# Optimization experiments

Measured on AMD Instinct MI355X. Metric: run time of the kernel, lower is better.

Reference implementation:

```python
import jax, jax.numpy as jnp
import numpy as np

EPS = 1e-5
SLOPE = 0.01  # torch LeakyReLU default

def _conv(x, w, b, stride):
    # x: [B,C,L], w: [O,I,3]
    y = jax.lax.conv_general_dilated(x, w, (stride,), [(1, 1)],
                                     dimension_numbers=("NCH", "OIH", "NCH"))
    return y + b[None, :, None]

def _bn(x, g, b, m, v):
    # eval-mode BatchNorm1d with running stats
    inv = jax.lax.rsqrt(v + EPS)
    return (x - m[None, :, None]) * (g * inv)[None, :, None] + b[None, :, None]

def _lrelu(x):
    return jnp.where(x >= 0, x, SLOPE * x)

def setup_inputs() -> dict:
    key = jax.random.key(0)
    ks = jax.random.split(key, 32)
    B, C, L = 32, 256, 2048
    K, D = 4096, 128
    d = {}
    d["x"] = jax.random.normal(ks[0], (B, C, L), dtype=jnp.float32)
    # conv weights [O,I,3]
    d["w1"] = jax.random.normal(ks[1], (256, 256, 3), jnp.float32) * 0.03
    d["b1"] = jax.random.normal(ks[2], (256,), jnp.float32) * 0.01
    d["w2"] = jax.random.normal(ks[3], (512, 256, 3), jnp.float32) * 0.03
    d["b2"] = jax.random.normal(ks[4], (512,), jnp.float32) * 0.01
    d["w3"] = jax.random.normal(ks[5], (512, 512, 3), jnp.float32) * 0.02
    d["b3"] = jax.random.normal(ks[6], (512,), jnp.float32) * 0.01
    d["w4"] = jax.random.normal(ks[7], (D, 512, 3), jnp.float32) * 0.02
    d["b4"] = jax.random.normal(ks[8], (D,), jnp.float32) * 0.01
    for i, ch in enumerate([256, 512, 512, D]):
        d[f"g{i+1}"] = 1.0 + 0.1 * jax.random.normal(ks[9 + 4 * i], (ch,), jnp.float32)
        d[f"be{i+1}"] = 0.1 * jax.random.normal(ks[10 + 4 * i], (ch,), jnp.float32)
        d[f"m{i+1}"] = 0.1 * jax.random.normal(ks[11 + 4 * i], (ch,), jnp.float32)
        d[f"v{i+1}"] = 0.5 + jax.random.uniform(ks[12 + 4 * i], (ch,), jnp.float32)
    d["emb"] = jax.random.uniform(ks[30], (K, D), jnp.float32,
                                  minval=-1.0 / K, maxval=1.0 / K)
    return d

def reference(x, w1, b1, w2, b2, w3, b3, w4, b4,
              g1, be1, m1, v1, g2, be2, m2, v2,
              g3, be3, m3, v3, g4, be4, m4, v4, emb):
    h = _lrelu(_bn(_conv(x, w1, b1, 2), g1, be1, m1, v1))   # [B,256,L/2]
    h = _lrelu(_bn(_conv(h, w2, b2, 2), g2, be2, m2, v2))   # [B,512,L/4]
    h = _lrelu(_bn(_conv(h, w3, b3, 2), g3, be3, m3, v3))   # [B,512,L/8]
    h = _lrelu(_bn(_conv(h, w4, b4, 1), g4, be4, m4, v4))   # [B,D,L/8]
    flat = jnp.transpose(h, (0, 2, 1)).reshape(-1, h.shape[1])  # [N,D]
    # squared-distance expansion: ||f||^2 + ||e||^2 - 2 f.e
    dist = (jnp.sum(flat * flat, axis=1, keepdims=True)
            + jnp.sum(emb * emb, axis=1)
            - 2.0 * flat @ emb.T)                            # [N,K]
    codes = jnp.argmin(dist, axis=1)
    return codes, dist
```

## Files before the change

kernel.cpp:

```cpp
#include <hip/hip_runtime.h>
#include <cstdint>
#include <math.h>

#define EPS_BN 1e-5f
#define SLOPE 0.01f
#define C14 6.103515625e-5f
#define SC14 16384.0f
#define HMIN 6.103515625e-5f

typedef __attribute__((ext_vector_type(8))) _Float16 half8;
typedef __attribute__((ext_vector_type(8))) short short8;
typedef __attribute__((ext_vector_type(16))) float f32x16;
typedef __attribute__((ext_vector_type(4))) float f32x4;

__device__ __forceinline__ void split16(float v, unsigned short& uh,
                                        unsigned short& ul) {
    _Float16 h = (_Float16)v;
    if (fabsf(v) < HMIN) h = (_Float16)0.0f;
    float rem = v - (float)h;
    _Float16 l = (_Float16)(rem * SC14);
    uh = __builtin_bit_cast(unsigned short, h);
    ul = __builtin_bit_cast(unsigned short, l);
}

typedef const __attribute__((address_space(1))) unsigned int* gas_ptr;
typedef __attribute__((address_space(3))) unsigned int* las_ptr;
__device__ __forceinline__ void glds16(const void* g, void* l) {
    __builtin_amdgcn_global_load_lds((gas_ptr)g, (las_ptr)l, 16, 0, 0);
}

__global__ __launch_bounds__(256)
void wprep_all(const float* __restrict__ w1, short* __restrict__ o1,
               const float* __restrict__ w2, short* __restrict__ o2,
               const float* __restrict__ w3, short* __restrict__ o3,
               const float* __restrict__ w4, short* __restrict__ o4)
{
    const float* w; short* wbuf; int CIN, COUT;
    switch (blockIdx.y) {
        case 0: w = w1; wbuf = o1; CIN = 256; COUT = 256; break;
        case 1: w = w2; wbuf = o2; CIN = 256; COUT = 512; break;
        case 2: w = w3; wbuf = o3; CIN = 512; COUT = 512; break;
        default: w = w4; wbuf = o4; CIN = 512; COUT = 128; break;
    }
    int KST = CIN / 16, OB = COUT / 128;
    int total = KST * OB * 1536;
    for (int sid = blockIdx.x * 256 + threadIdx.x; sid < total;
         sid += gridDim.x * 256) {
        int slot = sid % 1536;
        int kb = sid / 1536;
        int ob = kb % OB, ks = kb / OB;
        int m = slot & 31, hi = (slot >> 5) & 1, mf = (slot >> 6) & 3;
        int ts = slot >> 8;
        int t = ts >> 1, s = ts & 1;
        int oc = ob * 128 + mf * 32 + m;
        int ib = ks * 16 + hi * 8;
        short8 r;
        #pragma unroll
        for (int j = 0; j < 8; ++j) {
            float v = w[((size_t)oc * CIN + ib + j) * 3 + t];
            unsigned short uh, ul;
            split16(v, uh, ul);
            r[j] = (short)(s == 0 ? uh : ul);
        }
        *(short8*)(wbuf + (size_t)sid * 8) = r;
    }
}

__global__ __launch_bounds__(256)
void bnprep_init(
    const float* __restrict__ g1, const float* __restrict__ be1,
    const float* __restrict__ m1, const float* __restrict__ v1,
    const float* __restrict__ b1, float* __restrict__ sc1, float* __restrict__ off1,
    const float* __restrict__ g2, const float* __restrict__ be2,
    const float* __restrict__ m2, const float* __restrict__ v2,
    const float* __restrict__ b2, float* __restrict__ sc2, float* __restrict__ off2,
    const float* __restrict__ g3, const float* __restrict__ be3,
    const float* __restrict__ m3, const float* __restrict__ v3,
    const float* __restrict__ b3, float* __restrict__ sc3, float* __restrict__ off3,
    const float* __restrict__ g4, const float* __restrict__ be4,
    const float* __restrict__ m4, const float* __restrict__ v4,
    const float* __restrict__ b4, float* __restrict__ sc4, float* __restrict__ off4,
    unsigned long long* __restrict__ mp)
{
    int bid = blockIdx.x;
    if (bid >= 6) {
        mp[(bid - 6) * 256 + threadIdx.x] = ~0ULL;
        return;
    }
    const float *g, *be, *m, *v, *bias;
    float *sc, *off;
    int c;
    if (bid == 0) {
        g = g1; be = be1; m = m1; v = v1; bias = b1; sc = sc1; off = off1;
        c = threadIdx.x;
    } else if (bid <= 2) {
        g = g2; be = be2; m = m2; v = v2; bias = b2; sc = sc2; off = off2;
        c = (bid - 1) * 256 + threadIdx.x;
    } else if (bid <= 4) {
        g = g3; be = be3; m = m3; v = v3; bias = b3; sc = sc3; off = off3;
        c = (bid - 3) * 256 + threadIdx.x;
    } else {
        g = g4; be = be4; m = m4; v = v4; bias = b4; sc = sc4; off = off4;
        c = threadIdx.x;
        if (c >= 128) return;
    }
    float s = g[c] / sqrtf(v[c] + EPS_BN);
    sc[c] = s;
    off[c] = (bias[c] - m[c]) * s + be[c];
}

__global__ __launch_bounds__(256)
void xsplit(const float* __restrict__ x, short* __restrict__ xpl)
{
    const size_t PL = (size_t)32 * 32 * 2 * 1025 * 8;
    int l = blockIdx.x * 256 + threadIdx.x;
    int g = blockIdx.y, b = blockIdx.z;
    float v[8];
    #pragma unroll
    for (int j = 0; j < 8; ++j)
        v[j] = x[((size_t)b * 256 + g * 8 + j) * 2048 + l];
    int arr = l & 1;
    int slot = arr ? (l + 1) / 2 : l / 2 + 1;
    size_t base = ((((size_t)b * 32 + g) * 2 + arr) * 1025 + slot) * 8;
    short8 rh, rl;
    #pragma unroll
    for (int j = 0; j < 8; ++j) {
        unsigned short uh, ul;
        split16(v[j], uh, ul);
        rh[j] = (short)uh; rl[j] = (short)ul;
    }
    *(short8*)(xpl + base) = rh;
    *(short8*)(xpl + PL + base) = rl;
    if (l == 0) {
        short8 z;
        #pragma unroll
        for (int j = 0; j < 8; ++j) z[j] = 0;
        for (int sg = 0; sg < 2; ++sg)
            for (int a2 = 0; a2 < 2; ++a2)
                *(short8*)(xpl + sg * PL +
                           ((((size_t)b * 32 + g) * 2 + a2) * 1025) * 8) = z;
    }
}

template<int CIN, int COUT, int LIN, int STRIDE, int EPI>
__global__ __launch_bounds__(256, 2)
void conv_mfma(const short* __restrict__ wbuf, const short* __restrict__ xpl,
               const float* __restrict__ scv, const float* __restrict__ offv,
               short* __restrict__ opl, float* __restrict__ fout)
{
    constexpr int LOUT = LIN / STRIDE;
    constexpr int KST = CIN / 16;
    constexpr int OB = COUT / 128;
    constexpr int NG = CIN / 8;
    constexpr int NARR = (STRIDE == 2) ? 2 : 1;
    constexpr int SLOTS = (STRIDE == 2) ? (LIN / 2 + 1) : (LIN + 2);
    constexpr size_t PLIN = (size_t)32 * NG * NARR * SLOTS * 8;
    constexpr int NGo = COUT / 8;
    constexpr int OSLOTS = (EPI == 0) ? (LOUT / 2 + 1) : (LOUT + 2);
    constexpr size_t PLOUT = (size_t)32 * NGo * ((EPI == 0) ? 2 : 1) * OSLOTS * 8;

    constexpr int XOFF = 24576;
    constexpr int BUF  = 41472;
    constexpr int SCOFF = BUF;
    __shared__ __align__(16) char lds[BUF + 1024];

    const int tid = threadIdx.x;
    const int lane = tid & 63;
    const int wv = tid >> 6;
    const int wm = wv >> 1, wn = wv & 1;
    const int hi = lane >> 5, n32 = lane & 31;
    const int n0 = blockIdx.x * 128;
    const int ob = blockIdx.y;
    const int o0 = ob * 128;
    const int b = blockIdx.z;

    if (tid < 128) {
        ((float*)(lds + SCOFF))[tid] = scv[o0 + tid];
        ((float*)(lds + SCOFF + 512))[tid] = offv[o0 + tid];
    }

    f32x16 acc0[2][2], acc1[2][2];
    #pragma unroll
    for (int i = 0; i < 2; ++i)
        #pragma unroll
        for (int j = 0; j < 2; ++j)
            #pragma unroll
            for (int e = 0; e < 16; ++e) { acc0[i][j][e] = 0.0f; acc1[i][j][e] = 0.0f; }

    const short* wg = wbuf + (size_t)ob * 1536 * 8;
    const int lanexoff = hi * 4224 + n32 * 16;

    #pragma unroll 1
    for (int ks = 0; ks < KST; ++ks) {
        __syncthreads();
        {
            const short* wsrc = wg + (size_t)ks * OB * 1536 * 8;
            #pragma unroll
            for (int it = 0; it < 6; ++it) {
                int slot0 = it * 256 + wv * 64;
                glds16(wsrc + (size_t)(slot0 + lane) * 8, lds + slot0 * 16);
            }
        }
        {
            int g0 = ks * 2;
            constexpr int NRUNS = (STRIDE == 2) ? 8 : 4;
            for (int r = wv; r < NRUNS; r += 4) {
                int sg, rhi, arr, start, cnt;
                if (STRIDE == 2) {
                    sg = r >> 2; rhi = (r >> 1) & 1; arr = r & 1;
                    start = arr ? n0 : (n0 + 1);
                    cnt = arr ? 129 : 128;
                } else {
                    sg = r >> 1; rhi = r & 1; arr = 0;
                    start = n0; cnt = 130;
                }
                const short* src = xpl + (size_t)sg * PLIN
                    + ((((size_t)b * NG + (g0 + rhi)) * NARR + arr) * SLOTS + start) * 8;
                char* dst = lds + XOFF + ((sg * 2 + rhi) * 2 + arr) * 2112;
                for (int c0 = 0; c0 < cnt; c0 += 64) {
                    if (lane < cnt - c0)
                        glds16(src + (size_t)(c0 + lane) * 8, dst + c0 * 16);
                }
            }
        }
        __syncthreads();
        #pragma unroll
        for (int t = 0; t < 3; ++t) {
            half8 af[2][2], bx[2][2];
            #pragma unroll
            for (int s = 0; s < 2; ++s) {
                #pragma unroll
                for (int mf = 0; mf < 2; ++mf)
                    af[s][mf] = *(const half8*)(lds +
                        (((t * 2 + s) * 4 + (wm * 2 + mf)) * 64 + lane) * 16);
                #pragma unroll
                for (int nf = 0; nf < 2; ++nf) {
                    int arr, qb;
                    if (STRIDE == 2) {
                        arr = (t == 1) ? 0 : 1;
                        qb = wn * 64 + nf * 32 + ((t == 2) ? 1 : 0);
                    } else {
                        arr = 0;
                        qb = wn * 64 + nf * 32 + t;
                    }
                    bx[s][nf] = *(const half8*)(lds + XOFF + s * 8448
                                                + arr * 2112 + qb * 16 + lanexoff);
                }
            }
            #pragma unroll
            for (int mf = 0; mf < 2; ++mf)
                #pragma unroll
                for (int nf = 0; nf < 2; ++nf) {
                    acc0[mf][nf] = __builtin_amdgcn_mfma_f32_32x32x16_f16(
                        af[0][mf], bx[0][nf], acc0[mf][nf], 0, 0, 0);
                    acc1[mf][nf] = __builtin_amdgcn_mfma_f32_32x32x16_f16(
                        af[0][mf], bx[1][nf], acc1[mf][nf], 0, 0, 0);
                    acc1[mf][nf] = __builtin_amdgcn_mfma_f32_32x32x16_f16(
                        af[1][mf], bx[0][nf], acc1[mf][nf], 0, 0, 0);
                }
        }
    }

    #pragma unroll
    for (int half = 0; half < 2; ++half) {
        __syncthreads();
        #pragma unroll
        for (int mf = 0; mf < 2; ++mf)
            #pragma unroll
            for (int r = 0; r < 16; ++r) {
                int ocl = mf * 32 + (r & 3) + 8 * (r >> 2) + 4 * hi;
                *(float*)(lds + wv * 8704 + n32 * 272 + ocl * 4) =
                    acc0[mf][half][r] + C14 * acc1[mf][half][r];
            }
        __syncthreads();
        #pragma unroll
        for (int it = 0; it < 4; ++it) {
            int sl = tid + it * 256;
            int w = sl >> 8, rem = sl & 255, p = rem >> 3, grp = rem & 7;
            int wm_ = w >> 1, wn_ = w & 1;
            f32x4 v0 = *(f32x4*)(lds + w * 8704 + p * 272 + grp * 32);
            f32x4 v1 = *(f32x4*)(lds + w * 8704 + p * 272 + grp * 32 + 16);
            int oclb = wm_ * 64 + grp * 8;
            f32x4 s0 = *(f32x4*)(lds + SCOFF + oclb * 4);
            f32x4 s1 = *(f32x4*)(lds + SCOFF + oclb * 4 + 16);
            f32x4 q0 = *(f32x4*)(lds + SCOFF + 512 + oclb * 4);
            f32x4 q1 = *(f32x4*)(lds + SCOFF + 512 + oclb * 4 + 16);
            float y[8];
            #pragma unroll
            for (int j = 0; j < 4; ++j) {
                float a = v0[j] * s0[j] + q0[j];
                y[j] = a >= 0.0f ? a : SLOPE * a;
                float c = v1[j] * s1[j] + q1[j];
                y[4 + j] = c >= 0.0f ? c : SLOPE * c;
            }
            int pos_abs = n0 + wn_ * 64 + half * 32 + p;
            int oc_abs = o0 + oclb;
            if (EPI == 2) {
                f32x4 w0, w1;
                #pragma unroll
                for (int j = 0; j < 4; ++j) { w0[j] = y[j]; w1[j] = y[4 + j]; }
                float* fp = fout + ((size_t)(b * 256 + pos_abs)) * 128 + oc_abs;
                *(f32x4*)fp = w0;
                *(f32x4*)(fp + 4) = w1;
            } else {
                short8 rh, rl;
                #pragma unroll
                for (int j = 0; j < 8; ++j) {
                    unsigned short uh, ul;
                    split16(y[j], uh, ul);
                    rh[j] = (short)uh; rl[j] = (short)ul;
                }
                int gq = oc_abs >> 3;
                size_t base;
                if (EPI == 0) {
                    int arr = pos_abs & 1;
                    int slot = arr ? (pos_abs + 1) / 2 : pos_abs / 2 + 1;
                    base = ((((size_t)b * NGo + gq) * 2 + arr) * OSLOTS + slot) * 8;
                } else {
                    base = (((size_t)b * NGo + gq) * OSLOTS + (pos_abs + 1)) * 8;
                }
                *(short8*)(opl + base) = rh;
                *(short8*)(opl + PLOUT + base) = rl;
            }
        }
    }

    if (EPI == 0) {
        if (blockIdx.x == 0 && tid < 64) {
            int sg = tid / 32, r2 = tid % 32, g16 = r2 >> 1, a2 = r2 & 1;
            int gq = ob * 16 + g16;
            short8 z;
            #pragma unroll
            for (int j = 0; j < 8; ++j) z[j] = 0;
            *(short8*)(opl + (size_t)sg * PLOUT +
                       ((((size_t)b * NGo + gq) * 2 + a2) * OSLOTS) * 8) = z;
        }
    } else if (EPI == 1) {
        if (tid < 32 && (blockIdx.x == 0 || blockIdx.x == gridDim.x - 1)) {
            int sg = tid / 16, g16 = tid % 16;
            int gq = ob * 16 + g16;
            int slot = (blockIdx.x == 0) ? 0 : (OSLOTS - 1);
            short8 z;
            #pragma unroll
            for (int j = 0; j < 8; ++j) z[j] = 0;
            *(short8*)(opl + (size_t)sg * PLOUT +
                       (((size_t)b * NGo + gq) * OSLOTS + slot) * 8) = z;
        }
    }
}

__global__ __launch_bounds__(256)
void split_kernel(const float* __restrict__ src, int nrows,
                  short* __restrict__ ph, short* __restrict__ pl,
                  float* __restrict__ sumv)
{
    int t = blockIdx.x * 256 + threadIdx.x;
    int n = t >> 4, g = t & 15;
    if (n >= nrows) return;
    const float* rowp = src + (size_t)n * 128 + g * 8;
    float4 v0 = *(const float4*)rowp;
    float4 v1 = *(const float4*)(rowp + 4);
    float vv[8] = {v0.x, v0.y, v0.z, v0.w, v1.x, v1.y, v1.z, v1.w};
    short8 rh, rl;
    float ss = 0.0f;
    #pragma unroll
    for (int j = 0; j < 8; ++j) {
        float v = vv[j];
        ss = fmaf(v, v, ss);
        unsigned short uh, ul;
        split16(v, uh, ul);
        rh[j] = (short)uh; rl[j] = (short)ul;
    }
    int nb = n >> 5, m = n & 31, ks = g >> 1, hi = g & 1;
    size_t slot = ((((size_t)nb * 8 + ks) * 2 + hi) * 32 + m) * 8;
    *(short8*)(ph + slot) = rh;
    *(short8*)(pl + slot) = rl;
    #pragma unroll
    for (int mk = 8; mk; mk >>= 1) ss += __shfl_xor(ss, mk);
    if (g == 0) sumv[n] = ss;
}

__global__ __launch_bounds__(256, 2)
void distmin_kernel(const short* __restrict__ fh, const short* __restrict__ fl,
                    const short* __restrict__ eh, const short* __restrict__ el,
                    const float* __restrict__ sf, const float* __restrict__ se,
                    float* __restrict__ dist, unsigned long long* __restrict__ mp)
{
    __shared__ unsigned long long cand[128 * 64];
    const int tid = threadIdx.x;
    const int lane = tid & 63;
    const int wv = tid >> 6;
    const int wm = wv >> 1, wn = wv & 1;
    const int hi = lane >> 5, n32 = lane & 31;
    const int kb = blockIdx.x;
    const int nb = blockIdx.y;

    f32x16 acc0[2][2], acc1[2][2];
    #pragma unroll
    for (int i = 0; i < 2; ++i)
        #pragma unroll
        for (int j = 0; j < 2; ++j)
            #pragma unroll
            for (int e = 0; e < 16; ++e) { acc0[i][j][e] = 0.0f; acc1[i][j][e] = 0.0f; }

    const short* fb[2][2];
    const short* eb[2][2];
    {
        const short* fpl[2] = {fh, fl};
        const short* epl[2] = {eh, el};
        #pragma unroll
        for (int s = 0; s < 2; ++s) {
            #pragma unroll
            for (int mf = 0; mf < 2; ++mf)
                fb[s][mf] = fpl[s] + (size_t)nb * 16384
                            + ((size_t)(wm * 2 + mf) * 8 * 64 + lane) * 8;
            #pragma unroll
            for (int nf = 0; nf < 2; ++nf)
                eb[s][nf] = epl[s]
                            + ((size_t)(kb * 4 + wn * 2 + nf) * 8 * 64 + lane) * 8;
        }
    }

    #pragma unroll
    for (int ks = 0; ks < 8; ++ks) {
        half8 af[2][2], bx[2][2];
        #pragma unroll
        for (int s = 0; s < 2; ++s) {
            #pragma unroll
            for (int mf = 0; mf < 2; ++mf)
                af[s][mf] = *(const half8*)(fb[s][mf] + ks * 512);
            #pragma unroll
            for (int nf = 0; nf < 2; ++nf)
                bx[s][nf] = *(const half8*)(eb[s][nf] + ks * 512);
        }
        #pragma unroll
        for (int mf = 0; mf < 2; ++mf)
            #pragma unroll
            for (int nf = 0; nf < 2; ++nf) {
                acc0[mf][nf] = __builtin_amdgcn_mfma_f32_32x32x16_f16(
                    af[0][mf], bx[0][nf], acc0[mf][nf], 0, 0, 0);
                acc1[mf][nf] = __builtin_amdgcn_mfma_f32_32x32x16_f16(
                    af[0][mf], bx[1][nf], acc1[mf][nf], 0, 0, 0);
                acc1[mf][nf] = __builtin_amdgcn_mfma_f32_32x32x16_f16(
                    af[1][mf], bx[0][nf], acc1[mf][nf], 0, 0, 0);
            }
    }

    const int n_blk = nb * 128;
    const int kc0 = kb * 128 + wn * 64 + n32;
    const float se0 = se[kc0];
    const float se1 = se[kc0 + 32];
    #pragma unroll
    for (int mf = 0; mf < 2; ++mf) {
        #pragma unroll
        for (int r = 0; r < 16; ++r) {
            int nloc = wm * 64 + mf * 32 + (r & 3) + 8 * (r >> 2) + 4 * hi;
            int n = n_blk + nloc;
            float sfn = sf[n];
            float d0 = acc0[mf][0][r] + C14 * acc1[mf][0][r];
            float d1 = acc0[mf][1][r] + C14 * acc1[mf][1][r];
            float v0 = (sfn + se0) - 2.0f * d0;
            float v1 = (sfn + se1) - 2.0f * d1;
            dist[(size_t)n * 4096 + kc0] = v0;
            dist[(size_t)n * 4096 + kc0 + 32] = v1;
            unsigned long long p0 =
                (((unsigned long long)__float_as_uint(v0)) << 32) | (unsigned)kc0;
            unsigned long long p1 =
                (((unsigned long long)__float_as_uint(v1)) << 32) | (unsigned)(kc0 + 32);
            unsigned long long p = p1 < p0 ? p1 : p0;
            cand[nloc * 64 + wn * 32 + n32] = p;
        }
    }
    __syncthreads();
    {
        int row = tid >> 1, h = tid & 1;
        unsigned long long best = ~0ULL;
        #pragma unroll
        for (int i = 0; i < 32; ++i) {
            int c = h * 32 + ((i + row) & 31);
            unsigned long long cv = cand[row * 64 + c];
            best = cv < best ? cv : best;
        }
        unsigned lo = (unsigned)best, hw = (unsigned)(best >> 32);
        unsigned lo2 = __shfl_xor(lo, 1), hw2 = __shfl_xor(hw, 1);
        unsigned long long ob = (((unsigned long long)hw2) << 32) | lo2;
        if (ob < best) best = ob;
        if (h == 0) atomicMin(mp + n_blk + row, best);
    }
}

__global__ __launch_bounds__(256)
void codes_kernel(const unsigned long long* __restrict__ mp,
                  float* __restrict__ codes)
{
    int n = blockIdx.x * 256 + threadIdx.x;
    if (n < 8192) codes[n] = (float)(unsigned)(mp[n] & 0xffffffffULL);
}

extern "C" void kernel_launch(void* const* d_in, const int* in_sizes, int n_in,
                              void* d_out, int out_size, void* d_ws, size_t ws_size,
                              hipStream_t stream)
{
    const float* x   = (const float*)d_in[0];
    const float* w1  = (const float*)d_in[1];
    const float* b1  = (const float*)d_in[2];
    const float* w2  = (const float*)d_in[3];
    const float* b2  = (const float*)d_in[4];
    const float* w3  = (const float*)d_in[5];
    const float* b3  = (const float*)d_in[6];
    const float* w4  = (const float*)d_in[7];
    const float* b4  = (const float*)d_in[8];
    const float* g1  = (const float*)d_in[9];
    const float* be1 = (const float*)d_in[10];
    const float* m1  = (const float*)d_in[11];
    const float* v1  = (const float*)d_in[12];
    const float* g2  = (const float*)d_in[13];
    const float* be2 = (const float*)d_in[14];
    const float* m2  = (const float*)d_in[15];
    const float* v2  = (const float*)d_in[16];
    const float* g3  = (const float*)d_in[17];
    const float* be3 = (const float*)d_in[18];
    const float* m3  = (const float*)d_in[19];
    const float* v3  = (const float*)d_in[20];
    const float* g4  = (const float*)d_in[21];
    const float* be4 = (const float*)d_in[22];
    const float* m4  = (const float*)d_in[23];
    const float* v4  = (const float*)d_in[24];
    const float* emb = (const float*)d_in[25];

    float* outf  = (float*)d_out;
    float* codes = outf;
    float* distm = outf + 8192;

    char* wsb = (char*)d_ws;
    short* wb1 = (short*)(wsb + 0);
    short* wb2 = (short*)(wsb + 786432);
    short* wb3 = (short*)(wsb + 2359296);
    short* wb4 = (short*)(wsb + 5505024);
    float* sc1 = (float*)(wsb + 6291456); float* off1 = sc1 + 256;
    float* sc2 = (float*)(wsb + 6293504); float* off2 = sc2 + 512;
    float* sc3 = (float*)(wsb + 6297600); float* off3 = sc3 + 512;
    float* sc4 = (float*)(wsb + 6301696); float* off4 = sc4 + 128;
    short* h1p = (short*)(wsb + 6302720);
    short* fh  = (short*)(wsb + 39922688);
    short* fl  = (short*)(wsb + 42019840);
    short* eh  = (short*)(wsb + 44116992);
    short* el  = (short*)(wsb + 45165568);
    float* sf  = (float*)(wsb + 46214144);
    float* se  = (float*)(wsb + 46246912);
    unsigned long long* mp = (unsigned long long*)(wsb + 46263296);

    char* db = (char*)distm;
    short* xpl = (short*)db;
    short* h2p = (short*)db;
    short* h3p = (short*)(db + 33685504);
    float* f   = (float*)(db + 80000000);

    wprep_all<<<dim3(192, 4), 256, 0, stream>>>(w1, wb1, w2, wb2, w3, wb3, w4, wb4);
    bnprep_init<<<38, 256, 0, stream>>>(
        g1, be1, m1, v1, b1, sc1, off1,
        g2, be2, m2, v2, b2, sc2, off2,
        g3, be3, m3, v3, b3, sc3, off3,
        g4, be4, m4, v4, b4, sc4, off4, mp);
    split_kernel<<<256, 256, 0, stream>>>(emb, 4096, eh, el, se);

    xsplit<<<dim3(8, 32, 32), 256, 0, stream>>>(x, xpl);
    conv_mfma<256, 256, 2048, 2, 0>
        <<<dim3(8, 2, 32), 256, 0, stream>>>(wb1, xpl, sc1, off1, h1p, nullptr);
    conv_mfma<256, 512, 1024, 2, 0>
        <<<dim3(4, 4, 32), 256, 0, stream>>>(wb2, h1p, sc2, off2, h2p, nullptr);
    conv_mfma<512, 512, 512, 2, 1>
        <<<dim3(2, 4, 32), 256, 0, stream>>>(wb3, h2p, sc3, off3, h3p, nullptr);
    conv_mfma<512, 128, 256, 1, 2>
        <<<dim3(2, 1, 32), 256, 0, stream>>>(wb4, h3p, sc4, off4, nullptr, f);

    split_kernel<<<512, 256, 0, stream>>>(f, 8192, fh, fl, sf);
    distmin_kernel<<<dim3(32, 64), 256, 0, stream>>>(fh, fl, eh, el,
                                                     sf, se, distm, mp);
    codes_kernel<<<32, 256, 0, stream>>>(mp, codes);
}
```

Baseline: 263.5 us.

## Pair output-channel blocks in 512-thread conv blocks to share input tiles

```diff
diff --git a/kernel.cpp b/kernel.cpp
--- a/kernel.cpp
+++ b/kernel.cpp
@@ -142,22 +142,200 @@
     }
 }
 
-template<int CIN, int COUT, int LIN, int STRIDE, int EPI>
+template<int CIN, int COUT, int LIN, int TILE, int EPI>
+__global__ __launch_bounds__(512, 1)
+void conv_pair(const short* __restrict__ wbuf, const short* __restrict__ xpl,
+               const float* __restrict__ scv, const float* __restrict__ offv,
+               short* __restrict__ opl)
+{
+    constexpr int LOUT = LIN / 2;
+    constexpr int KST = CIN / 16;
+    constexpr int OBS = COUT / 128;
+    constexpr int NG = CIN / 8;
+    constexpr int SLOTS = LIN / 2 + 1;
+    constexpr size_t PLIN = (size_t)32 * NG * 2 * SLOTS * 8;
+    constexpr int NF = TILE / 64;
+    constexpr int NGo = COUT / 8;
+    constexpr int OSLOTS = (EPI == 0) ? (LOUT / 2 + 1) : (LOUT + 2);
+    constexpr size_t PLOUT = (size_t)32 * NGo * ((EPI == 0) ? 2 : 1) * OSLOTS * 8;
+
+    constexpr int XOFF = 49152;
+    constexpr int SCOFF = 69632;
+    __shared__ __align__(16) char lds[71680];
+
+    const int tid = threadIdx.x;
+    const int lane = tid & 63;
+    const int wv = tid >> 6;
+    const int wo = wv >> 2;
+    const int wm = (wv >> 1) & 1, wn = wv & 1;
+    const int hi = lane >> 5, n32 = lane & 31;
+    const int n0 = blockIdx.x * TILE;
+    const int oby = blockIdx.y;
+    const int o0 = oby * 256;
+    const int b = blockIdx.z;
+
+    if (tid < 256) ((float*)(lds + SCOFF))[tid] = scv[o0 + tid];
+    else ((float*)(lds + SCOFF + 1024))[tid - 256] = offv[o0 + tid - 256];
+
+    f32x16 acc0[2][2], acc1[2][2];
+    #pragma unroll
+    for (int i = 0; i < 2; ++i)
+        #pragma unroll
+        for (int j = 0; j < 2; ++j)
+            #pragma unroll
+            for (int e = 0; e < 16; ++e) { acc0[i][j][e] = 0.0f; acc1[i][j][e] = 0.0f; }
+
+    #pragma unroll 1
+    for (int ks = 0; ks < KST; ++ks) {
+        __syncthreads();
+        {
+            const short* wsrc = wbuf +
+                ((size_t)ks * OBS + (oby * 2 + wo)) * 1536 * 8;
+            #pragma unroll
+            for (int it = 0; it < 6; ++it) {
+                int slot0 = it * 256 + (wv & 3) * 64;
+                glds16(wsrc + (size_t)(slot0 + lane) * 8,
+                       lds + wo * 24576 + slot0 * 16);
+            }
+        }
+        {
+            int g0 = ks * 2;
+            int r = wv;
+            int sg = r >> 2, rhi = (r >> 1) & 1, arr = r & 1;
+            int start = arr ? n0 : (n0 + 1);
+            int cnt = arr ? (TILE + 1) : TILE;
+            const short* src = xpl + (size_t)sg * PLIN
+                + ((((size_t)b * NG + (g0 + rhi)) * 2 + arr) * SLOTS + start) * 8;
+            char* dst = lds + XOFF + ((sg * 2 + rhi) * 2 + arr) * 2112;
+            for (int c0 = 0; c0 < cnt; c0 += 64) {
+                if (lane < cnt - c0)
+                    glds16(src + (size_t)(c0 + lane) * 8, dst + c0 * 16);
+            }
+        }
+        __syncthreads();
+        #pragma unroll
+        for (int t = 0; t < 3; ++t) {
+            half8 af[2][2], bx[2][2];
+            #pragma unroll
+            for (int s = 0; s < 2; ++s) {
+                #pragma unroll
+                for (int mf = 0; mf < 2; ++mf)
+                    af[s][mf] = *(const half8*)(lds + wo * 24576 +
+                        (((t * 2 + s) * 4 + (wm * 2 + mf)) * 64 + lane) * 16);
+                int arr = (t == 1) ? 0 : 1;
+                int tof = (t == 2) ? 1 : 0;
+                #pragma unroll
+                for (int nf = 0; nf < NF; ++nf) {
+                    int qb = wn * (TILE / 2) + nf * 32 + tof;
+                    bx[s][nf] = *(const half8*)(lds + XOFF + s * 8448
+                                                + arr * 2112 + qb * 16
+                                                + hi * 4224 + n32 * 16);
+                }
+            }
+            #pragma unroll
+            for (int mf = 0; mf < 2; ++mf)
+                #pragma unroll
+                for (int nf = 0; nf < NF; ++nf) {
+                    acc0[mf][nf] = __builtin_amdgcn_mfma_f32_32x32x16_f16(
+                        af[0][mf], bx[0][nf], acc0[mf][nf], 0, 0, 0);
+                    acc1[mf][nf] = __builtin_amdgcn_mfma_f32_32x32x16_f16(
+                        af[0][mf], bx[1][nf], acc1[mf][nf], 0, 0, 0);
+                    acc1[mf][nf] = __builtin_amdgcn_mfma_f32_32x32x16_f16(
+                        af[1][mf], bx[0][nf], acc1[mf][nf], 0, 0, 0);
+                }
+        }
+    }
+
+    #pragma unroll
+    for (int half = 0; half < NF; ++half) {
+        __syncthreads();
+        #pragma unroll
+        for (int mf = 0; mf < 2; ++mf)
+            #pragma unroll
+            for (int r = 0; r < 16; ++r) {
+                int ocl = mf * 32 + (r & 3) + 8 * (r >> 2) + 4 * hi;
+                *(float*)(lds + wv * 8704 + n32 * 272 + ocl * 4) =
+                    acc0[mf][half][r] + C14 * acc1[mf][half][r];
+            }
+        __syncthreads();
+        #pragma unroll
+        for (int it = 0; it < 4; ++it) {
+            int sl = tid + it * 512;
+            int w = sl >> 8, rem = sl & 255, p = rem >> 3, grp = rem & 7;
+            int wo_ = w >> 2, wm_ = (w >> 1) & 1, wn_ = w & 1;
+            f32x4 v0 = *(f32x4*)(lds + w * 8704 + p * 272 + grp * 32);
+            f32x4 v1 = *(f32x4*)(lds + w * 8704 + p * 272 + grp * 32 + 16);
+            int ocb = wo_ * 128 + wm_ * 64 + grp * 8;
+            f32x4 s0 = *(f32x4*)(lds + SCOFF + ocb * 4);
+            f32x4 s1 = *(f32x4*)(lds + SCOFF + ocb * 4 + 16);
+            f32x4 q0 = *(f32x4*)(lds + SCOFF + 1024 + ocb * 4);
+            f32x4 q1 = *(f32x4*)(lds + SCOFF + 1024 + ocb * 4 + 16);
+            float y[8];
+            #pragma unroll
+            for (int j = 0; j < 4; ++j) {
+                float a = v0[j] * s0[j] + q0[j];
+                y[j] = a >= 0.0f ? a : SLOPE * a;
+                float c = v1[j] * s1[j] + q1[j];
+                y[4 + j] = c >= 0.0f ? c : SLOPE * c;
+            }
+            int pos_abs = n0 + wn_ * (TILE / 2) + half * 32 + p;
+            int oc_abs = o0 + ocb;
+            short8 rh, rl;
+            #pragma unroll
+            for (int j = 0; j < 8; ++j) {
+                unsigned short uh, ul;
+                split16(y[j], uh, ul);
+                rh[j] = (short)uh; rl[j] = (short)ul;
+            }
+            int gq = oc_abs >> 3;
+            size_t base;
+            if (EPI == 0) {
+                int arr = pos_abs & 1;
+                int slot = arr ? (pos_abs + 1) / 2 : pos_abs / 2 + 1;
+                base = ((((size_t)b * NGo + gq) * 2 + arr) * OSLOTS + slot) * 8;
+            } else {
+                base = (((size_t)b * NGo + gq) * OSLOTS + (pos_abs + 1)) * 8;
+            }
+            *(short8*)(opl + base) = rh;
+            *(short8*)(opl + PLOUT + base) = rl;
+        }
+    }
+
+    if (EPI == 0) {
+        if (blockIdx.x == 0 && tid < 128) {
+            int sg = tid >> 6, r2 = tid & 63, g16 = r2 >> 1, a2 = r2 & 1;
+            int gq = oby * 32 + g16;
+            short8 z;
+            #pragma unroll
+            for (int j = 0; j < 8; ++j) z[j] = 0;
+            *(short8*)(opl + (size_t)sg * PLOUT +
+                       ((((size_t)b * NGo + gq) * 2 + a2) * OSLOTS) * 8) = z;
+        }
+    } else {
+        if (tid < 64 && (blockIdx.x == 0 || blockIdx.x == gridDim.x - 1)) {
+            int sg = tid >> 5, g16 = tid & 31;
+            int gq = oby * 32 + g16;
+            int slot = (blockIdx.x == 0) ? 0 : (OSLOTS - 1);
+            short8 z;
+            #pragma unroll
+            for (int j = 0; j < 8; ++j) z[j] = 0;
+            *(short8*)(opl + (size_t)sg * PLOUT +
+                       (((size_t)b * NGo + gq) * OSLOTS + slot) * 8) = z;
+        }
+    }
+}
+
+template<int CIN, int COUT, int LIN>
 __global__ __launch_bounds__(256, 2)
-void conv_mfma(const short* __restrict__ wbuf, const short* __restrict__ xpl,
-               const float* __restrict__ scv, const float* __restrict__ offv,
-               short* __restrict__ opl, float* __restrict__ fout)
-{
-    constexpr int LOUT = LIN / STRIDE;
+void conv_s1(const short* __restrict__ wbuf, const short* __restrict__ xpl,
+             const float* __restrict__ scv, const float* __restrict__ offv,
+             float* __restrict__ fout)
+{
     constexpr int KST = CIN / 16;
     constexpr int OB = COUT / 128;
     constexpr int NG = CIN / 8;
-    constexpr int NARR = (STRIDE == 2) ? 2 : 1;
-    constexpr int SLOTS = (STRIDE == 2) ? (LIN / 2 + 1) : (LIN + 2);
-    constexpr size_t PLIN = (size_t)32 * NG * NARR * SLOTS * 8;
-    constexpr int NGo = COUT / 8;
-    constexpr int OSLOTS = (EPI == 0) ? (LOUT / 2 + 1) : (LOUT + 2);
-    constexpr size_t PLOUT = (size_t)32 * NGo * ((EPI == 0) ? 2 : 1) * OSLOTS * 8;
+    constexpr int SLOTS = LIN + 2;
+    constexpr size_t PLIN = (size_t)32 * NG * SLOTS * 8;
 
     constexpr int XOFF = 24576;
     constexpr int BUF  = 41472;
@@ -203,22 +381,13 @@
         }
         {
             int g0 = ks * 2;
-            constexpr int NRUNS = (STRIDE == 2) ? 8 : 4;
-            for (int r = wv; r < NRUNS; r += 4) {
-                int sg, rhi, arr, start, cnt;
-                if (STRIDE == 2) {
-                    sg = r >> 2; rhi = (r >> 1) & 1; arr = r & 1;
-                    start = arr ? n0 : (n0 + 1);
-                    cnt = arr ? 129 : 128;
-                } else {
-                    sg = r >> 1; rhi = r & 1; arr = 0;
-                    start = n0; cnt = 130;
-                }
+            for (int r = wv; r < 4; r += 4) {
+                int sg = r >> 1, rhi = r & 1;
                 const short* src = xpl + (size_t)sg * PLIN
-                    + ((((size_t)b * NG + (g0 + rhi)) * NARR + arr) * SLOTS + start) * 8;
-                char* dst = lds + XOFF + ((sg * 2 + rhi) * 2 + arr) * 2112;
-                for (int c0 = 0; c0 < cnt; c0 += 64) {
-                    if (lane < cnt - c0)
+                    + (((size_t)b * NG + (g0 + rhi)) * SLOTS + n0) * 8;
+                char* dst = lds + XOFF + (sg * 2 + rhi) * 2112;
+                for (int c0 = 0; c0 < 130; c0 += 64) {
+                    if (lane < 130 - c0)
                         glds16(src + (size_t)(c0 + lane) * 8, dst + c0 * 16);
                 }
             }
@@ -235,16 +404,9 @@
                         (((t * 2 + s) * 4 + (wm * 2 + mf)) * 64 + lane) * 16);
                 #pragma unroll
                 for (int nf = 0; nf < 2; ++nf) {
-                    int arr, qb;
-                    if (STRIDE == 2) {
-                        arr = (t == 1) ? 0 : 1;
-                        qb = wn * 64 + nf * 32 + ((t == 2) ? 1 : 0);
-                    } else {
-                        arr = 0;
-                        qb = wn * 64 + nf * 32 + t;
-                    }
-                    bx[s][nf] = *(const half8*)(lds + XOFF + s * 8448
-                                                + arr * 2112 + qb * 16 + lanexoff);
+                    int qb = wn * 64 + nf * 32 + t;
+                    bx[s][nf] = *(const half8*)(lds + XOFF + s * 4224
+                                                + qb * 16 + hi * 2112 + n32 * 16);
                 }
             }
             #pragma unroll
@@ -285,66 +447,18 @@
             f32x4 s1 = *(f32x4*)(lds + SCOFF + oclb * 4 + 16);
             f32x4 q0 = *(f32x4*)(lds + SCOFF + 512 + oclb * 4);
             f32x4 q1 = *(f32x4*)(lds + SCOFF + 512 + oclb * 4 + 16);
-            float y[8];
+            f32x4 w0, w1;
             #pragma unroll
             for (int j = 0; j < 4; ++j) {
                 float a = v0[j] * s0[j] + q0[j];
-                y[j] = a >= 0.0f ? a : SLOPE * a;
+                w0[j] = a >= 0.0f ? a : SLOPE * a;
                 float c = v1[j] * s1[j] + q1[j];
-                y[4 + j] = c >= 0.0f ? c : SLOPE * c;
+                w1[j] = c >= 0.0f ? c : SLOPE * c;
             }
             int pos_abs = n0 + wn_ * 64 + half * 32 + p;
-            int oc_abs = o0 + oclb;
-            if (EPI == 2) {
-                f32x4 w0, w1;
-                #pragma unroll
-                for (int j = 0; j < 4; ++j) { w0[j] = y[j]; w1[j] = y[4 + j]; }
-                float* fp = fout + ((size_t)(b * 256 + pos_abs)) * 128 + oc_abs;
-                *(f32x4*)fp = w0;
-                *(f32x4*)(fp + 4) = w1;
-            } else {
-                short8 rh, rl;
-                #pragma unroll
-                for (int j = 0; j < 8; ++j) {
-                    unsigned short uh, ul;
-                    split16(y[j], uh, ul);
-                    rh[j] = (short)uh; rl[j] = (short)ul;
-                }
-                int gq = oc_abs >> 3;
-                size_t base;
-                if (EPI == 0) {
-                    int arr = pos_abs & 1;
-                    int slot = arr ? (pos_abs + 1) / 2 : pos_abs / 2 + 1;
-                    base = ((((size_t)b * NGo + gq) * 2 + arr) * OSLOTS + slot) * 8;
-                } else {
-                    base = (((size_t)b * NGo + gq) * OSLOTS + (pos_abs + 1)) * 8;
-                }
-                *(short8*)(opl + base) = rh;
-                *(short8*)(opl + PLOUT + base) = rl;
-            }
-        }
-    }
-
-    if (EPI == 0) {
-        if (blockIdx.x == 0 && tid < 64) {
-            int sg = tid / 32, r2 = tid % 32, g16 = r2 >> 1, a2 = r2 & 1;
-            int gq = ob * 16 + g16;
-            short8 z;
-            #pragma unroll
-            for (int j = 0; j < 8; ++j) z[j] = 0;
-            *(short8*)(opl + (size_t)sg * PLOUT +
-                       ((((size_t)b * NGo + gq) * 2 + a2) * OSLOTS) * 8) = z;
-        }
-    } else if (EPI == 1) {
-        if (tid < 32 && (blockIdx.x == 0 || blockIdx.x == gridDim.x - 1)) {
-            int sg = tid / 16, g16 = tid % 16;
-            int gq = ob * 16 + g16;
-            int slot = (blockIdx.x == 0) ? 0 : (OSLOTS - 1);
-            short8 z;
-            #pragma unroll
-            for (int j = 0; j < 8; ++j) z[j] = 0;
-            *(short8*)(opl + (size_t)sg * PLOUT +
-                       (((size_t)b * NGo + gq) * OSLOTS + slot) * 8) = z;
+            float* fp = fout + ((size_t)(b * 256 + pos_abs)) * 128 + o0 + oclb;
+            *(f32x4*)fp = w0;
+            *(f32x4*)(fp + 4) = w1;
         }
     }
 }
@@ -461,8 +575,8 @@
             float d1 = acc0[mf][1][r] + C14 * acc1[mf][1][r];
             float v0 = (sfn + se0) - 2.0f * d0;
             float v1 = (sfn + se1) - 2.0f * d1;
-            dist[(size_t)n * 4096 + kc0] = v0;
-            dist[(size_t)n * 4096 + kc0 + 32] = v1;
+            __builtin_nontemporal_store(v0, &dist[(size_t)n * 4096 + kc0]);
+            __builtin_nontemporal_store(v1, &dist[(size_t)n * 4096 + kc0 + 32]);
             unsigned long long p0 =
                 (((unsigned long long)__float_as_uint(v0)) << 32) | (unsigned)kc0;
             unsigned long long p1 =
@@ -565,14 +679,14 @@
     split_kernel<<<256, 256, 0, stream>>>(emb, 4096, eh, el, se);
 
     xsplit<<<dim3(8, 32, 32), 256, 0, stream>>>(x, xpl);
-    conv_mfma<256, 256, 2048, 2, 0>
-        <<<dim3(8, 2, 32), 256, 0, stream>>>(wb1, xpl, sc1, off1, h1p, nullptr);
-    conv_mfma<256, 512, 1024, 2, 0>
-        <<<dim3(4, 4, 32), 256, 0, stream>>>(wb2, h1p, sc2, off2, h2p, nullptr);
-    conv_mfma<512, 512, 512, 2, 1>
-        <<<dim3(2, 4, 32), 256, 0, stream>>>(wb3, h2p, sc3, off3, h3p, nullptr);
-    conv_mfma<512, 128, 256, 1, 2>
-        <<<dim3(2, 1, 32), 256, 0, stream>>>(wb4, h3p, sc4, off4, nullptr, f);
+    conv_pair<256, 256, 2048, 128, 0>
+        <<<dim3(8, 1, 32), 512, 0, stream>>>(wb1, xpl, sc1, off1, h1p);
+    conv_pair<256, 512, 1024, 128, 0>
+        <<<dim3(4, 2, 32), 512, 0, stream>>>(wb2, h1p, sc2, off2, h2p);
+    conv_pair<512, 512, 512, 64, 1>
+        <<<dim3(4, 2, 32), 512, 0, stream>>>(wb3, h2p, sc3, off3, h3p);
+    conv_s1<512, 128, 256>
+        <<<dim3(2, 1, 32), 256, 0, stream>>>(wb4, h3p, sc4, off4, f);
 
     split_kernel<<<512, 256, 0, stream>>>(f, 8192, fh, fl, sf);
     distmin_kernel<<<dim3(32, 64), 256, 0, stream>>>(fh, fl, eh, el,
```

Result: no change. 263.8 us (+0.1%).
